# Kernel tuning notes

Hardware: AMD Instinct MI355X
Metric: run time of the kernel (lower is better)

The kernel has to match this reference:

```python
import jax, jax.numpy as jnp
import numpy as np

H = 256  # rnn_size


def setup_inputs() -> dict:
    key = jax.random.key(0)
    ks = jax.random.split(key, 6)
    B, T, F, D = 64, 512, 64, 64
    s_in = 1.0 / np.sqrt(F)
    s_rec = 1.0 / np.sqrt(H)
    return {
        "x": jax.random.normal(ks[0], (B, T, F), jnp.float32),
        "kernel": jax.random.normal(ks[1], (F, 3 * H), jnp.float32) * s_in,
        "recurrent_kernel": jax.random.normal(ks[2], (H, 3 * H), jnp.float32) * s_rec,
        "bias": jax.random.normal(ks[3], (3 * H,), jnp.float32) * 0.01,
        "dense_w": jax.random.normal(ks[4], (H, D), jnp.float32) * s_rec,
        "dense_b": jax.random.normal(ks[5], (D,), jnp.float32) * 0.01,
    }


def _gru_scan(x, kernel, recurrent_kernel, bias):
    B, T, _ = x.shape
    # Pre-project all timesteps: [B, T, 3H]
    xproj = jnp.einsum("btf,fg->btg", x, kernel) + bias
    xproj_t = jnp.transpose(xproj, (1, 0, 2))  # [T, B, 3H]

    def step(h, xt):
        # Keras GRU, reset_after=False: r gates the recurrent matmul of the candidate
        rec = h @ recurrent_kernel  # [B, 3H]
        xz, xr, xh = xt[:, :H], xt[:, H:2 * H], xt[:, 2 * H:]
        rz, rr, rh = rec[:, :H], rec[:, H:2 * H], rec[:, 2 * H:]
        z = jax.nn.sigmoid(xz + rz)
        r = jax.nn.sigmoid(xr + rr)
        hh = jnp.tanh(xh + r * rh)
        h_new = z * h + (1.0 - z) * hh
        return h_new, h_new

    h0 = jnp.zeros((B, H), x.dtype)
    h_last, outs = jax.lax.scan(step, h0, xproj_t)
    return jnp.transpose(outs, (1, 0, 2)), h_last  # [B,T,H], [B,H]


def reference(x, kernel, recurrent_kernel, bias, dense_w, dense_b):
    outputs, h_last = _gru_scan(x, kernel, recurrent_kernel, bias)
    state = jnp.tanh(h_last @ dense_w + dense_b)  # [B, dense_size]
    return outputs, state
```

## Files before the change

kernel.cpp:

```cpp
#include <hip/hip_runtime.h>


typedef _Float16 half2_t __attribute__((ext_vector_type(2)));
typedef _Float16 f16x4_t __attribute__((ext_vector_type(4)));
typedef _Float16 f16x8_t __attribute__((ext_vector_type(8)));
typedef float f32x4_t __attribute__((ext_vector_type(4)));

#define LOG2E 1.4426950408889634f

__device__ __forceinline__ float fast_sigmoid(float x) {
  float e = __builtin_amdgcn_exp2f(-x * LOG2E);
  return __builtin_amdgcn_rcpf(1.0f + e);
}
__device__ __forceinline__ float fast_tanh(float x) {
  float e = __builtin_amdgcn_exp2f(x * (2.0f * LOG2E));
  return 1.0f - 2.0f * __builtin_amdgcn_rcpf(1.0f + e);
}

__global__ __launch_bounds__(256, 4) void xproj_gemm(
    const float* __restrict__ x, const float* __restrict__ kmat,
    const float* __restrict__ bias, _Float16* __restrict__ xp) {
  __shared__ half2_t As2[32][132];
  __shared__ half2_t Bs2[32][132];
  const int tid = threadIdx.x;
  const int rb = blockIdx.x * 128;
  const int cb = blockIdx.y * 128;

  {
    const int k4 = (tid & 15) * 4;
    const int r0 = tid >> 4;
#pragma unroll
    for (int p = 0; p < 8; ++p) {
      int r = r0 + p * 16;
      float4 v = *(const float4*)(x + (size_t)(rb + r) * 64 + k4);
      half2_t lo, hi;
      lo[0] = (_Float16)v.x; lo[1] = (_Float16)v.y;
      hi[0] = (_Float16)v.z; hi[1] = (_Float16)v.w;
      As2[k4 / 2][r] = lo;
      As2[k4 / 2 + 1][r] = hi;
    }
  }
  {
    const int c4 = (tid & 31) * 4;
    const int kp0 = tid >> 5;
#pragma unroll
    for (int p = 0; p < 4; ++p) {
      int kp = kp0 + p * 8;
      float4 va = *(const float4*)(kmat + (size_t)(2 * kp) * 768 + cb + c4);
      float4 vb = *(const float4*)(kmat + (size_t)(2 * kp + 1) * 768 + cb + c4);
      half2_t o0, o1, o2, o3;
      o0[0] = (_Float16)va.x; o0[1] = (_Float16)vb.x;
      o1[0] = (_Float16)va.y; o1[1] = (_Float16)vb.y;
      o2[0] = (_Float16)va.z; o2[1] = (_Float16)vb.z;
      o3[0] = (_Float16)va.w; o3[1] = (_Float16)vb.w;
      Bs2[kp][c4 + 0] = o0;
      Bs2[kp][c4 + 1] = o1;
      Bs2[kp][c4 + 2] = o2;
      Bs2[kp][c4 + 3] = o3;
    }
  }
  __syncthreads();

  const int tx = tid & 15, ty = tid >> 4;
  const int r0 = ty * 8;
  const int c0 = tx * 4;
  float acc[8][8];
  {
    float4 b0 = *(const float4*)(bias + cb + c0);
    float4 b1 = *(const float4*)(bias + cb + 64 + c0);
    float bz[8] = {b0.x, b0.y, b0.z, b0.w, b1.x, b1.y, b1.z, b1.w};
#pragma unroll
    for (int i = 0; i < 8; ++i)
#pragma unroll
      for (int j = 0; j < 8; ++j) acc[i][j] = bz[j];
  }

#pragma unroll 2
  for (int kp = 0; kp < 32; ++kp) {
    half2_t a2[8], b2[8];
    *(int4*)(&a2[0]) = *(const int4*)(&As2[kp][r0]);
    *(int4*)(&a2[4]) = *(const int4*)(&As2[kp][r0 + 4]);
    *(int2*)(&b2[0]) = *(const int2*)(&Bs2[kp][c0]);
    *(int2*)(&b2[2]) = *(const int2*)(&Bs2[kp][c0 + 2]);
    *(int2*)(&b2[4]) = *(const int2*)(&Bs2[kp][64 + c0]);
    *(int2*)(&b2[6]) = *(const int2*)(&Bs2[kp][64 + c0 + 2]);
#pragma unroll
    for (int i = 0; i < 8; ++i)
#pragma unroll
      for (int j = 0; j < 8; ++j)
        acc[i][j] = __builtin_amdgcn_fdot2(a2[i], b2[j], acc[i][j], false);
  }

#pragma unroll
  for (int i = 0; i < 8; ++i) {
    f16x4_t o0, o1;
#pragma unroll
    for (int j = 0; j < 4; ++j) {
      o0[j] = (_Float16)acc[i][j];
      o1[j] = (_Float16)acc[i][4 + j];
    }
    _Float16* dst = xp + (size_t)(rb + r0 + i) * 768 + cb;
    *(f16x4_t*)(dst + c0) = o0;
    *(f16x4_t*)(dst + 64 + c0) = o1;
  }
}

__global__ __launch_bounds__(1024, 4) void gru_scan(
    const _Float16* __restrict__ xp, const float* __restrict__ wr,
    const float* __restrict__ dw, const float* __restrict__ db,
    float* __restrict__ out, float* __restrict__ state) {
  __shared__ alignas(16) _Float16 zz[256];
  __shared__ alignas(16) _Float16 hh0[256];
  __shared__ alignas(16) _Float16 hh1[256];
  __shared__ float hbuf[256];

  const int tid = threadIdx.x;
  const int b = blockIdx.x;
  const int lane = tid & 63;
  const int w = tid >> 6;
  const int q = lane >> 4;
  const int col = w * 16 + (lane & 15);
  const bool gl = (lane < 16);

  f16x8_t wf[3][8];
#pragma unroll
  for (int g = 0; g < 3; ++g)
#pragma unroll
    for (int s = 0; s < 8; ++s) {
      const float* wp = wr + (size_t)(s * 32 + q * 8) * 768 + g * 256 + col;
      f16x8_t v;
#pragma unroll
      for (int j = 0; j < 8; ++j) v[j] = (_Float16)wp[(size_t)j * 768];
      wf[g][s] = v;
    }

  if (tid < 256) {
    zz[tid] = (_Float16)0.0f;
    hh0[tid] = (_Float16)0.0f;
  }
  __syncthreads();

  const bool arow0 = ((lane & 15) == 0);
  const _Float16* ab0 = (arow0 ? hh0 : zz) + q * 8;
  const _Float16* ab1 = (arow0 ? hh1 : zz) + q * 8;

  const _Float16* xpb = xp + (size_t)b * 512 * 768;
  float* outb = out + (size_t)b * 512 * 256;
  float hprev = 0.0f;

#pragma unroll 2
  for (int t = 0; t < 512; ++t) {
    const _Float16* ab = (t & 1) ? ab1 : ab0;
    _Float16* hw = (t & 1) ? hh0 : hh1;

    _Float16 xz = (_Float16)0.0f, xr = (_Float16)0.0f, xh = (_Float16)0.0f;
    if (gl) {
      if (t) outb[(size_t)(t - 1) * 256 + col] = hprev;
      const _Float16* xq = xpb + (size_t)t * 768 + col;
      xz = xq[0];
      xr = xq[256];
      xh = xq[512];
    }

    f32x4_t az = {0.f, 0.f, 0.f, 0.f};
    f32x4_t ar = {0.f, 0.f, 0.f, 0.f};
    f32x4_t ah = {0.f, 0.f, 0.f, 0.f};
#pragma unroll
    for (int s = 0; s < 8; ++s) {
      f16x8_t a = *(const f16x8_t*)(ab + s * 32);
      az = __builtin_amdgcn_mfma_f32_16x16x32_f16(a, wf[0][s], az, 0, 0, 0);
      ar = __builtin_amdgcn_mfma_f32_16x16x32_f16(a, wf[1][s], ar, 0, 0, 0);
      ah = __builtin_amdgcn_mfma_f32_16x16x32_f16(a, wf[2][s], ah, 0, 0, 0);
    }

    if (gl) {
      float z = fast_sigmoid((float)xz + az[0]);
      float r = fast_sigmoid((float)xr + ar[0]);
      float hcand = fast_tanh((float)xh + r * ah[0]);
      float hnew = z * hprev + (1.0f - z) * hcand;
      hprev = hnew;
      hw[col] = (_Float16)hnew;
    }
    __syncthreads();
  }

  if (gl) {
    outb[(size_t)511 * 256 + col] = hprev;
    hbuf[col] = hprev;
  }
  __syncthreads();

  if (tid < 64) {
    float acc = db[tid];
#pragma unroll 8
    for (int k = 0; k < 256; ++k) acc = fmaf(hbuf[k], dw[k * 64 + tid], acc);
    state[(size_t)b * 64 + tid] = fast_tanh(acc);
  }
}

extern "C" void kernel_launch(void* const* d_in, const int* in_sizes, int n_in,
                              void* d_out, int out_size, void* d_ws,
                              size_t ws_size, hipStream_t stream) {
  const float* x = (const float*)d_in[0];
  const float* kmat = (const float*)d_in[1];
  const float* wr = (const float*)d_in[2];
  const float* bias = (const float*)d_in[3];
  const float* dw = (const float*)d_in[4];
  const float* db = (const float*)d_in[5];

  float* out = (float*)d_out;
  float* state = out + (size_t)64 * 512 * 256;
  _Float16* xp = (_Float16*)d_ws;

  dim3 gg(32768 / 128, 768 / 128);
  xproj_gemm<<<gg, 256, 0, stream>>>(x, kmat, bias, xp);
  gru_scan<<<64, 1024, 0, stream>>>(xp, wr, dw, db, out, state);
}
```

Baseline: 733.9 us.

## Batch 16 sequences per GRU scan block using full MFMA rows

Previously each block handled one batch row and used only row 0 of the 16-row MFMA tile, leaving the other fifteen rows as zeros. Each block now processes 16 batch rows, with all MFMA output rows active, and the launch shrinks from 64 blocks to 4. Hidden states are held in an XOR-swizzled shared buffer to avoid bank conflicts, and all lanes do the gate math for four rows. This fills the matrix units but uses only 4 CUs, so the serial per-step latency (gate math, global x loads and output stores now spread over all lanes) decides whether it helps.

```diff
diff --git a/kernel.cpp b/kernel.cpp
--- a/kernel.cpp
+++ b/kernel.cpp
@@ -109,92 +109,109 @@
     const _Float16* __restrict__ xp, const float* __restrict__ wr,
     const float* __restrict__ dw, const float* __restrict__ db,
     float* __restrict__ out, float* __restrict__ state) {
-  __shared__ alignas(16) _Float16 zz[256];
-  __shared__ alignas(16) _Float16 hh0[256];
-  __shared__ alignas(16) _Float16 hh1[256];
-  __shared__ float hbuf[256];
+  __shared__ alignas(16) _Float16 hh[2 * 16 * 256];
+  __shared__ float hF[16 * 256];
 
   const int tid = threadIdx.x;
-  const int b = blockIdx.x;
+  const int bg = blockIdx.x;
   const int lane = tid & 63;
   const int w = tid >> 6;
-  const int q = lane >> 4;
-  const int col = w * 16 + (lane & 15);
-  const bool gl = (lane < 16);
+  const int lq = lane >> 4;
+  const int b15 = lane & 15;
+  const int colw = w * 16 + b15;
 
   f16x8_t wf[3][8];
 #pragma unroll
   for (int g = 0; g < 3; ++g)
 #pragma unroll
     for (int s = 0; s < 8; ++s) {
-      const float* wp = wr + (size_t)(s * 32 + q * 8) * 768 + g * 256 + col;
+      const float* wp = wr + (size_t)(s * 32 + lq * 8) * 768 + g * 256 + colw;
       f16x8_t v;
 #pragma unroll
       for (int j = 0; j < 8; ++j) v[j] = (_Float16)wp[(size_t)j * 768];
       wf[g][s] = v;
     }
 
-  if (tid < 256) {
-    zz[tid] = (_Float16)0.0f;
-    hh0[tid] = (_Float16)0.0f;
-  }
+  {
+    int2 z2;
+    z2.x = 0;
+    z2.y = 0;
+    ((int2*)hh)[tid] = z2;
+  }
+
+  int a_addr[8];
+#pragma unroll
+  for (int s = 0; s < 8; ++s)
+    a_addr[s] = b15 * 512 + (((s * 4 + lq) ^ b15) << 4);
+
+  int w_addr[4];
+  uint px[4], po[4];
+#pragma unroll
+  for (int r = 0; r < 4; ++r) {
+    const int br = lq * 4 + r;
+    w_addr[r] = br * 512 + (((colw >> 3) ^ br) << 4) + ((colw & 7) << 1);
+    px[r] = ((uint)(bg * 16 + br) * (512u * 768u) + (uint)colw) * 2u;
+    po[r] = ((uint)(bg * 16 + br) * (512u * 256u) + (uint)colw) * 4u;
+  }
+  const char* xpc = (const char*)xp;
+  char* outc = (char*)out;
+
+  float hp[4] = {0.0f, 0.0f, 0.0f, 0.0f};
   __syncthreads();
 
-  const bool arow0 = ((lane & 15) == 0);
-  const _Float16* ab0 = (arow0 ? hh0 : zz) + q * 8;
-  const _Float16* ab1 = (arow0 ? hh1 : zz) + q * 8;
-
-  const _Float16* xpb = xp + (size_t)b * 512 * 768;
-  float* outb = out + (size_t)b * 512 * 256;
-  float hprev = 0.0f;
-
-#pragma unroll 2
-  for (int t = 0; t < 512; ++t) {
-    const _Float16* ab = (t & 1) ? ab1 : ab0;
-    _Float16* hw = (t & 1) ? hh0 : hh1;
-
-    _Float16 xz = (_Float16)0.0f, xr = (_Float16)0.0f, xh = (_Float16)0.0f;
-    if (gl) {
-      if (t) outb[(size_t)(t - 1) * 256 + col] = hprev;
-      const _Float16* xq = xpb + (size_t)t * 768 + col;
-      xz = xq[0];
-      xr = xq[256];
-      xh = xq[512];
-    }
-
-    f32x4_t az = {0.f, 0.f, 0.f, 0.f};
-    f32x4_t ar = {0.f, 0.f, 0.f, 0.f};
-    f32x4_t ah = {0.f, 0.f, 0.f, 0.f};
-#pragma unroll
-    for (int s = 0; s < 8; ++s) {
-      f16x8_t a = *(const f16x8_t*)(ab + s * 32);
-      az = __builtin_amdgcn_mfma_f32_16x16x32_f16(a, wf[0][s], az, 0, 0, 0);
-      ar = __builtin_amdgcn_mfma_f32_16x16x32_f16(a, wf[1][s], ar, 0, 0, 0);
-      ah = __builtin_amdgcn_mfma_f32_16x16x32_f16(a, wf[2][s], ah, 0, 0, 0);
-    }
-
-    if (gl) {
-      float z = fast_sigmoid((float)xz + az[0]);
-      float r = fast_sigmoid((float)xr + ar[0]);
-      float hcand = fast_tanh((float)xh + r * ah[0]);
-      float hnew = z * hprev + (1.0f - z) * hcand;
-      hprev = hnew;
-      hw[col] = (_Float16)hnew;
-    }
-    __syncthreads();
-  }
-
-  if (gl) {
-    outb[(size_t)511 * 256 + col] = hprev;
-    hbuf[col] = hprev;
+#define GSTEP(T, RD, WR)                                                    \
+  {                                                                         \
+    const uint xo = (uint)(T)*1536u;                                        \
+    _Float16 xz[4], xr[4], xh[4];                                           \
+    _Pragma("unroll") for (int r = 0; r < 4; ++r) {                         \
+      const _Float16* xq = (const _Float16*)(xpc + (px[r] + xo));           \
+      xz[r] = xq[0];                                                        \
+      xr[r] = xq[256];                                                      \
+      xh[r] = xq[512];                                                      \
+    }                                                                       \
+    f32x4_t az = {0.f, 0.f, 0.f, 0.f};                                      \
+    f32x4_t ar = {0.f, 0.f, 0.f, 0.f};                                      \
+    f32x4_t ah = {0.f, 0.f, 0.f, 0.f};                                      \
+    _Pragma("unroll") for (int s = 0; s < 8; ++s) {                         \
+      f16x8_t a = *(const f16x8_t*)((const char*)hh + (RD) + a_addr[s]);    \
+      az = __builtin_amdgcn_mfma_f32_16x16x32_f16(a, wf[0][s], az, 0, 0, 0);\
+      ar = __builtin_amdgcn_mfma_f32_16x16x32_f16(a, wf[1][s], ar, 0, 0, 0);\
+      ah = __builtin_amdgcn_mfma_f32_16x16x32_f16(a, wf[2][s], ah, 0, 0, 0);\
+    }                                                                       \
+    _Pragma("unroll") for (int r = 0; r < 4; ++r) {                         \
+      if ((T) > 0)                                                          \
+        *(float*)(outc + (po[r] + ((uint)(T)-1u) * 1024u)) = hp[r];         \
+      float z = fast_sigmoid((float)xz[r] + az[r]);                         \
+      float rg = fast_sigmoid((float)xr[r] + ar[r]);                        \
+      float hc = fast_tanh((float)xh[r] + rg * ah[r]);                      \
+      hp[r] = hc + z * (hp[r] - hc);                                        \
+      *(_Float16*)((char*)hh + (WR) + w_addr[r]) = (_Float16)hp[r];         \
+    }                                                                       \
+    __syncthreads();                                                        \
+  }
+
+#pragma unroll 1
+  for (int tt = 0; tt < 512; tt += 2) {
+    GSTEP(tt, 0, 8192)
+    GSTEP(tt + 1, 8192, 0)
+  }
+#undef GSTEP
+
+#pragma unroll
+  for (int r = 0; r < 4; ++r) {
+    *(float*)(outc + (po[r] + 511u * 1024u)) = hp[r];
+    hF[(lq * 4 + r) * 256 + colw] = hp[r];
   }
   __syncthreads();
 
-  if (tid < 64) {
-    float acc = db[tid];
+  {
+    const int bt = tid >> 6;
+    const int d = lane;
+    float acc = db[d];
 #pragma unroll 8
-    for (int k = 0; k < 256; ++k) acc = fmaf(hbuf[k], dw[k * 64 + tid], acc);
-    state[(size_t)b * 64 + tid] = fast_tanh(acc);
+    for (int k = 0; k < 256; ++k)
+      acc = fmaf(hF[bt * 256 + k], dw[k * 64 + d], acc);
+    state[(size_t)(bg * 16 + bt) * 64 + d] = fast_tanh(acc);
   }
 }
 
@@ -214,5 +231,5 @@
 
   dim3 gg(32768 / 128, 768 / 128);
   xproj_gemm<<<gg, 256, 0, stream>>>(x, kmat, bias, xp);
-  gru_scan<<<64, 1024, 0, stream>>>(xp, wr, dw, db, out, state);
-}
+  gru_scan<<<4, 1024, 0, stream>>>(xp, wr, dw, db, out, state);
+}
```

Result: slower. 2.341 ms (+219.0%).
